# Optimization experiments

Hardware: AMD Instinct MI355X
Metric: run time of the kernel (lower is better)

Reference implementation:

```python
import jax, jax.numpy as jnp
import numpy as np

H = 256  # hidden_size


def _lstm_cell(x, h, c, Wih, Whh, b):
    # PyTorch gate order: input, forget, cell(g), output
    gates = x @ Wih.T + h @ Whh.T + b  # (B, 4H)
    i, f, g, o = jnp.split(gates, 4, axis=-1)
    c_new = jax.nn.sigmoid(f) * c + jax.nn.sigmoid(i) * jnp.tanh(g)
    h_new = jax.nn.sigmoid(o) * jnp.tanh(c_new)
    return h_new, c_new


def setup_inputs() -> dict:
    key = jax.random.key(0)
    ks = jax.random.split(key, 9)
    B, D_in, T, H4 = 64, 64, 1024, 4 * H
    s = 0.05  # keep gates out of saturation
    return {
        "x": jax.random.normal(ks[0], (B, D_in, T), jnp.float32),
        # layer 0: input size 64; layers 1-2: input size 2*H (bidirectional concat)
        "Wih0": jax.random.normal(ks[1], (2, H4, D_in), jnp.float32) * s,
        "Whh0": jax.random.normal(ks[2], (2, H4, H), jnp.float32) * s,
        "b0": jax.random.normal(ks[3], (2, H4), jnp.float32) * s,  # b_ih + b_hh fused
        "Wih12": jax.random.normal(ks[4], (2, 2, H4, 2 * H), jnp.float32) * s,
        "Whh12": jax.random.normal(ks[5], (2, 2, H4, H), jnp.float32) * s,
        "b12": jax.random.normal(ks[6], (2, 2, H4), jnp.float32) * s,
        # Conv1d(1, 81, (256,1)) == per-timestep linear over the hidden dim
        "conv_w": jax.random.normal(ks[7], (81, H), jnp.float32) * s,
        "conv_b": jax.random.normal(ks[8], (81,), jnp.float32) * s,
    }


def reference(x, Wih0, Whh0, b0, Wih12, Whh12, b12, conv_w, conv_b):
    B = x.shape[0]
    seq = jnp.transpose(x, (2, 0, 1))  # (T, B, D_in) like x.permute(2,0,1)
    h0 = jnp.zeros((6, B, H), x.dtype)  # num_layers * num_directions = 6
    c0 = jnp.zeros((6, B, H), x.dtype)

    def step(carry, x_t):
        h, c = carry
        hs, cs = [], []
        inp = x_t  # single timestep fed to the (bi)LSTM: both dirs see the same input
        for l in range(3):
            outs = []
            for d in range(2):
                idx = 2 * l + d
                if l == 0:
                    Wih, Whh, b = Wih0[d], Whh0[d], b0[d]
                else:
                    Wih, Whh, b = Wih12[l - 1, d], Whh12[l - 1, d], b12[l - 1, d]
                hn, cn = _lstm_cell(inp, h[idx], c[idx], Wih, Whh, b)
                outs.append(hn)
                hs.append(hn)
                cs.append(cn)
            inp = jnp.concatenate(outs, axis=-1)  # (B, 2H) into next layer
        new_h = jnp.stack(hs)
        new_c = jnp.stack(cs)
        # h.view(L, 2, B, H)[-1, -1]: last layer, backward direction
        return (new_h, new_c), hs[-1]

    _, ys = jax.lax.scan(step, (h0, c0), seq)  # ys: (T, B, H)

    # y.permute(1,2,0).unsqueeze(1) -> conv (256,1) kernel -> squeeze(2):
    # logits[b, o, t] = sum_h conv_w[o, h] * ys[t, b, h] + conv_b[o]
    logits = jnp.einsum('tbh,oh->bot', ys, conv_w) + conv_b[None, :, None]
    probs = jax.nn.softmax(logits, axis=1)
    return jnp.argmax(probs, axis=1)  # (B, T) int
```

## Files before the change

kernel.cpp:

```cpp
#include <hip/hip_runtime.h>


#define H_ 256
#define B_ 64
#define T_ 1024
#define NBLK 256
#define NTHR 1024
#define HBUF 98304
#define NTICK 1026

#define OFF_GEN  0
#define OFF_ROOT 64
#define OFF_CNT  128
#define OFF_H    4096
#define OFF_XT   1048576
#define OFF_YS   17825792

__device__ __forceinline__ float sigf(float x) {
  return 1.0f / (1.0f + __expf(-x));
}
__device__ __forceinline__ float tanhf_(float x) {
  float e = __expf(-2.0f * fabsf(x));
  float r = (1.0f - e) / (1.0f + e);
  return x >= 0.0f ? r : -r;
}

__device__ __forceinline__ void llc_ld1(const float4* p, float4& r) {
  asm volatile(
      "global_load_dwordx4 %0, %1, off sc0 sc1\n\t"
      "s_waitcnt vmcnt(0)"
      : "=v"(r)
      : "v"(p)
      : "memory");
}
__device__ __forceinline__ void llc_ld4(const float4* p, float4& r0, float4& r1,
                                        float4& r2, float4& r3) {
  asm volatile(
      "global_load_dwordx4 %0, %4, off sc0 sc1\n\t"
      "global_load_dwordx4 %1, %4, off offset:1024 sc0 sc1\n\t"
      "global_load_dwordx4 %2, %4, off offset:2048 sc0 sc1\n\t"
      "global_load_dwordx4 %3, %4, off offset:3072 sc0 sc1\n\t"
      "s_waitcnt vmcnt(0)"
      : "=&v"(r0), "=&v"(r1), "=&v"(r2), "=&v"(r3)
      : "v"(p)
      : "memory");
}
__device__ __forceinline__ void llc_st1(float* p, float v) {
  asm volatile(
      "global_store_dword %0, %1, off sc0 sc1\n\t"
      "s_waitcnt vmcnt(0)" ::"v"(p),
      "v"(v)
      : "memory");
}
__device__ __forceinline__ void llc_st2(float* p1, float v1, float* p2, float v2) {
  asm volatile(
      "global_store_dword %0, %1, off sc0 sc1\n\t"
      "global_store_dword %2, %3, off sc0 sc1\n\t"
      "s_waitcnt vmcnt(0)" ::"v"(p1),
      "v"(v1), "v"(p2), "v"(v2)
      : "memory");
}

__global__ __launch_bounds__(64) void transpose_x(const float* __restrict__ x,
                                                  float* __restrict__ xT) {
  __shared__ float tile[64][65];
  const int k = blockIdx.y;
  const int t0 = blockIdx.x * 64;
  const int lane = threadIdx.x;
  for (int bi = 0; bi < 64; ++bi)
    tile[bi][lane] = x[bi * 65536 + k * 1024 + t0 + lane];
  __syncthreads();
  for (int ti = 0; ti < 64; ++ti)
    xT[(size_t)(t0 + ti) * 4096 + (k >> 2) * 256 + lane * 4 + (k & 3)] =
        tile[lane][ti];
}

__device__ __forceinline__ void body8(float* __restrict__ acc, const float4 av,
                                      const float* __restrict__ wl,
                                      const int k4) {
  const float* wp = wl + (size_t)k4 * 32;
#pragma unroll
  for (int a = 0; a < 8; ++a) {
    float4 wq = *(const float4*)(wp + a * 4);
    acc[a] += wq.x * av.x + wq.y * av.y + wq.z * av.z + wq.w * av.w;
  }
}

__device__ __forceinline__ void seg8(float* __restrict__ acc, const int a,
                                     const int b, const float4* __restrict__ act,
                                     const int actOff,
                                     const float* __restrict__ wl,
                                     const int lane, const bool byp) {
  int k4 = a;
  for (; k4 + 4 <= b; k4 += 4) {
    const float4* p = act + (size_t)(k4 - actOff) * 64 + lane;
    float4 v0, v1, v2, v3;
    if (byp) {
      llc_ld4(p, v0, v1, v2, v3);
    } else {
      v0 = p[0];
      v1 = p[64];
      v2 = p[128];
      v3 = p[192];
    }
    body8(acc, v0, wl, k4 + 0);
    body8(acc, v1, wl, k4 + 1);
    body8(acc, v2, wl, k4 + 2);
    body8(acc, v3, wl, k4 + 3);
  }
  for (; k4 < b; ++k4) {
    const float4* p = act + (size_t)(k4 - actOff) * 64 + lane;
    float4 v;
    if (byp)
      llc_ld1(p, v);
    else
      v = *p;
    body8(acc, v, wl, k4);
  }
}

__device__ __forceinline__ void task8(
    const int w, const int lane, const int tid, const int u0,
    const int K4, const int nA4,
    const float4* __restrict__ actA, const bool bypA,
    const float4* __restrict__ actB, const bool bypB,
    const float* __restrict__ wl,
    const float* __restrict__ bias,
    float* __restrict__ cst2,
    float* __restrict__ hcell,
    float* __restrict__ ysrow,
    float (*red)[64][12], const bool lastTask) {
  const int slice = K4 >> 4;
  const int lo = w * slice, hi = lo + slice;
  float acc[8] = {0.f, 0.f, 0.f, 0.f, 0.f, 0.f, 0.f, 0.f};

  {
    const int b4 = hi < nA4 ? hi : nA4;
    if (lo < b4) seg8(acc, lo, b4, actA, 0, wl, lane, bypA);
  }
  {
    const int a4 = lo > nA4 ? lo : nA4;
    if (a4 < hi) seg8(acc, a4, hi, actB, nA4, wl, lane, bypB);
  }

  *(float4*)&red[w][lane][0] = make_float4(acc[0], acc[1], acc[2], acc[3]);
  *(float4*)&red[w][lane][4] = make_float4(acc[4], acc[5], acc[6], acc[7]);
  __syncthreads();

  if (tid < 128) {
    const int uu = tid >> 6, b = tid & 63;
    float gi = bias[0 * 256 + u0 + uu];
    float gf = bias[1 * 256 + u0 + uu];
    float gg = bias[2 * 256 + u0 + uu];
    float go = bias[3 * 256 + u0 + uu];
#pragma unroll
    for (int ww = 0; ww < 16; ++ww) {
      float4 s = *(const float4*)&red[ww][b][uu * 4];
      gi += s.x; gf += s.y; gg += s.z; go += s.w;
    }
    float iv = sigf(gi), fv = sigf(gf), gv = tanhf_(gg), ov = sigf(go);
    float c = fv * cst2[uu * 64 + b] + iv * gv;
    cst2[uu * 64 + b] = c;
    float h = ov * tanhf_(c);
    const int u = u0 + uu;
    float* hp = hcell + (u >> 2) * 256 + b * 4 + (u & 3);
    if (ysrow)
      llc_st2(hp, h, ysrow + b * 256 + u, h);
    else
      llc_st1(hp, h);
  }
  if (!lastTask) __syncthreads();
}

__global__ __launch_bounds__(NTHR, 1) void lstm_persistent(
    const float* __restrict__ Wih0, const float* __restrict__ Whh0,
    const float* __restrict__ b0, const float* __restrict__ Wih12,
    const float* __restrict__ Whh12, const float* __restrict__ b12, char* wsb) {
  unsigned* gen = (unsigned*)(wsb + OFF_GEN);
  unsigned* root = (unsigned*)(wsb + OFF_ROOT);
  float* hb = (float*)(wsb + OFF_H);
  const float* xT = (const float*)(wsb + OFF_XT);
  float* ys = (float*)(wsb + OFF_YS);

  __shared__ float red[16][64][12];
  __shared__ float cst[3][2][64];
  __shared__ float wlds[14848];

  const int bid = blockIdx.x;
  const int tid = threadIdx.x;
  const int lane = tid & 63;
  const int w = __builtin_amdgcn_readfirstlane(tid >> 6);
  const int d = bid >> 7;
  const int u0 = (bid & 127) * 2;

  if (tid < 384) ((float*)cst)[tid] = 0.f;

  auto stage = [&](const float* wA, int wAs, const float* wB, int wBs,
                   int K4s, int NA4s, float* dst) {
    const int nq = K4s * 8;
    for (int idx = tid; idx < nq; idx += NTHR) {
      const int a = idx / K4s;
      const int k4 = idx - a * K4s;
      const int row = (a & 3) * 256 + u0 + (a >> 2);
      const float* src = (k4 < NA4s) ? (wA + (size_t)row * wAs + k4 * 4)
                                     : (wB + (size_t)row * wBs + (k4 - NA4s) * 4);
      float4 q = *(const float4*)src;
      *(float4*)(dst + ((size_t)k4 * 8 + a) * 4) = q;
    }
  };
  stage(Wih0 + (size_t)d * 65536, 64, Whh0 + (size_t)d * 262144, 256, 80, 16,
        wlds);
  stage(Wih12 + (size_t)d * 524288, 512, Whh12 + (size_t)d * 262144, 256, 192,
        128, wlds + 2560);
  stage(Wih12 + (size_t)(2 + d) * 524288, 512,
        Whh12 + (size_t)(2 + d) * 262144, 256, 192, 128, wlds + 8704);
  __syncthreads();

  unsigned* mycnt = (unsigned*)(wsb + OFF_CNT + (size_t)(bid & 7) * 64);

  for (unsigned tick = 0; tick < NTICK; ++tick) {
    const float* R = hb + ((tick + 1) & 1) * HBUF;
    float* W = hb + (tick & 1) * HBUF;
    const float4* Rf4 = (const float4*)R;

    const bool has0 = tick < 1024;
    const bool has1 = tick >= 1 && tick < 1025;
    const bool has2 = tick >= 2;

    if (has0) {
      task8(w, lane, tid, u0, 80, 16,
            (const float4*)xT + (size_t)tick * 1024, false,
            Rf4 + (size_t)d * 4096, true,
            wlds, b0 + d * 1024, &cst[0][0][0],
            W + (size_t)d * 16384, nullptr, red, !(has1 || has2));
    }
    if (has1) {
      task8(w, lane, tid, u0, 192, 128,
            Rf4, true,
            Rf4 + (size_t)(2 + d) * 4096, true,
            wlds + 2560, b12 + d * 1024, &cst[1][0][0],
            W + (size_t)(2 + d) * 16384, nullptr, red, !has2);
    }
    if (has2) {
      const int t = (int)tick - 2;
      task8(w, lane, tid, u0, 192, 128,
            Rf4 + (size_t)2 * 4096, true,
            Rf4 + (size_t)(4 + d) * 4096, true,
            wlds + 8704, b12 + (2 + d) * 1024, &cst[2][0][0],
            W + (size_t)(4 + d) * 16384,
            (d == 1) ? (ys + (size_t)t * 16384) : nullptr, red, true);
    }

    __syncthreads();
    if (tid == 0) {
      unsigned old = __hip_atomic_fetch_add(mycnt, 1u, __ATOMIC_RELAXED,
                                            __HIP_MEMORY_SCOPE_AGENT);
      if (old == (tick + 1) * (NBLK / 8) - 1) {
        unsigned r = __hip_atomic_fetch_add(root, 1u, __ATOMIC_RELAXED,
                                            __HIP_MEMORY_SCOPE_AGENT);
        if (r == (tick + 1) * 8 - 1) {
          __hip_atomic_store(gen, tick + 1, __ATOMIC_RELAXED,
                             __HIP_MEMORY_SCOPE_AGENT);
        }
      }
      while (__hip_atomic_load(gen, __ATOMIC_RELAXED, __HIP_MEMORY_SCOPE_AGENT) <
             tick + 1) {
        __builtin_amdgcn_s_sleep(2);
      }
    }
    __syncthreads();
  }
}

__global__ __launch_bounds__(256) void conv_argmax(const float* __restrict__ yst,
                                                   const float* __restrict__ cw,
                                                   const float* __restrict__ cb,
                                                   int* __restrict__ out) {
  const int t = blockIdx.x;
  const int tid = threadIdx.x, lane = tid & 63, w = tid >> 6;
  const float* yrow = yst + (size_t)t * (B_ * H_) + lane * H_;
  float best = -3.4e38f;
  int bi = 0;
  for (int og = 0; og < 3; ++og) {
    float acc[8];
    int ov[8];
#pragma unroll
    for (int m = 0; m < 8; ++m) {
      int o = w + 32 * og + 4 * m;
      ov[m] = (o < 81) ? o : 80;
      acc[m] = (o < 81) ? cb[o] : -3.4e38f;
    }
    for (int uu = 0; uu < H_; uu += 4) {
      float4 y4 = *(const float4*)(yrow + uu);
#pragma unroll
      for (int m = 0; m < 8; ++m) {
        const float* wr = cw + ov[m] * H_ + uu;
        acc[m] += wr[0] * y4.x + wr[1] * y4.y + wr[2] * y4.z + wr[3] * y4.w;
      }
    }
#pragma unroll
    for (int m = 0; m < 8; ++m) {
      int o = w + 32 * og + 4 * m;
      if (o < 81 && acc[m] > best) {
        best = acc[m];
        bi = o;
      }
    }
  }
  __shared__ float sv[4][64];
  __shared__ int si[4][64];
  sv[w][lane] = best;
  si[w][lane] = bi;
  __syncthreads();
  if (tid < 64) {
    float bv = sv[0][tid];
    int bo = si[0][tid];
#pragma unroll
    for (int ww = 1; ww < 4; ++ww) {
      float v = sv[ww][tid];
      int o = si[ww][tid];
      if (v > bv || (v == bv && o < bo)) {
        bv = v;
        bo = o;
      }
    }
    out[tid * T_ + t] = bo;
  }
}

extern "C" void kernel_launch(void* const* d_in, const int* in_sizes, int n_in,
                              void* d_out, int out_size, void* d_ws,
                              size_t ws_size, hipStream_t stream) {
  const float* x = (const float*)d_in[0];
  const float* Wih0 = (const float*)d_in[1];
  const float* Whh0 = (const float*)d_in[2];
  const float* b0 = (const float*)d_in[3];
  const float* Wih12 = (const float*)d_in[4];
  const float* Whh12 = (const float*)d_in[5];
  const float* b12 = (const float*)d_in[6];
  const float* cw = (const float*)d_in[7];
  const float* cb = (const float*)d_in[8];
  int* out = (int*)d_out;
  char* wsb = (char*)d_ws;

  hipMemsetAsync(wsb, 0, OFF_H + 786432, stream);
  transpose_x<<<dim3(16, 64, 1), dim3(64, 1, 1), 0, stream>>>(
      x, (float*)(wsb + OFF_XT));
  lstm_persistent<<<dim3(NBLK, 1, 1), dim3(NTHR, 1, 1), 0, stream>>>(
      Wih0, Whh0, b0, Wih12, Whh12, b12, wsb);
  conv_argmax<<<dim3(T_, 1, 1), dim3(256, 1, 1), 0, stream>>>(
      (const float*)(wsb + OFF_YS), cw, cb, out);
}
```

Measured before the change: 18.34 ms.

## Run three LSTM layer cells concurrently across warp groups per tick

Instead of running the three layer cells one after another, each with its own block-wide reduction and barrier, the 16 warps are split into groups: 4 for layer 0 and 6 each for layers 1 and 2. All three matvecs now run at once, followed by a single shared reduction and pointwise phase handled by 192 threads. This removes two __syncthreads per tick and shortens the serial per-tick path. It also adds 8-wide bypass loads, caches the biases in LDS, and packs the two hidden-unit stores into one dwordx2 store. The cost is uneven work per warp, since layer-0 warps have less K to cover.

```diff
diff --git a/kernel.cpp b/kernel.cpp
--- a/kernel.cpp
+++ b/kernel.cpp
@@ -45,20 +45,28 @@
       : "v"(p)
       : "memory");
 }
-__device__ __forceinline__ void llc_st1(float* p, float v) {
+__device__ __forceinline__ void llc_ld8(const float4* p, const float4* q,
+                                        float4& r0, float4& r1, float4& r2,
+                                        float4& r3, float4& r4, float4& r5,
+                                        float4& r6, float4& r7) {
   asm volatile(
-      "global_store_dword %0, %1, off sc0 sc1\n\t"
-      "s_waitcnt vmcnt(0)" ::"v"(p),
-      "v"(v)
+      "global_load_dwordx4 %0, %8, off sc0 sc1\n\t"
+      "global_load_dwordx4 %1, %8, off offset:1024 sc0 sc1\n\t"
+      "global_load_dwordx4 %2, %8, off offset:2048 sc0 sc1\n\t"
+      "global_load_dwordx4 %3, %8, off offset:3072 sc0 sc1\n\t"
+      "global_load_dwordx4 %4, %9, off sc0 sc1\n\t"
+      "global_load_dwordx4 %5, %9, off offset:1024 sc0 sc1\n\t"
+      "global_load_dwordx4 %6, %9, off offset:2048 sc0 sc1\n\t"
+      "global_load_dwordx4 %7, %9, off offset:3072 sc0 sc1\n\t"
+      "s_waitcnt vmcnt(0)"
+      : "=&v"(r0), "=&v"(r1), "=&v"(r2), "=&v"(r3), "=&v"(r4), "=&v"(r5),
+        "=&v"(r6), "=&v"(r7)
+      : "v"(p), "v"(q)
       : "memory");
 }
-__device__ __forceinline__ void llc_st2(float* p1, float v1, float* p2, float v2) {
-  asm volatile(
-      "global_store_dword %0, %1, off sc0 sc1\n\t"
-      "global_store_dword %2, %3, off sc0 sc1\n\t"
-      "s_waitcnt vmcnt(0)" ::"v"(p1),
-      "v"(v1), "v"(p2), "v"(v2)
-      : "memory");
+__device__ __forceinline__ void llc_st_f2(float* p, float2 v) {
+  asm volatile("global_store_dwordx2 %0, %1, off sc0 sc1" ::"v"(p), "v"(v)
+               : "memory");
 }
 
 __global__ __launch_bounds__(64) void transpose_x(const float* __restrict__ x,
@@ -86,90 +94,65 @@
   }
 }
 
-__device__ __forceinline__ void seg8(float* __restrict__ acc, const int a,
-                                     const int b, const float4* __restrict__ act,
-                                     const int actOff,
-                                     const float* __restrict__ wl,
-                                     const int lane, const bool byp) {
-  int k4 = a;
-  for (; k4 + 4 <= b; k4 += 4) {
-    const float4* p = act + (size_t)(k4 - actOff) * 64 + lane;
+__device__ __forceinline__ void runLLC(float* __restrict__ acc,
+                                       const float4* __restrict__ bufbase,
+                                       const int bufk4, const int wk4,
+                                       const int n,
+                                       const float* __restrict__ wl,
+                                       const int lane) {
+  const float4* p = bufbase + (size_t)bufk4 * 64 + lane;
+  int k = 0;
+  for (; k + 8 <= n; k += 8) {
+    float4 v0, v1, v2, v3, v4, v5, v6, v7;
+    llc_ld8(p, p + 256, v0, v1, v2, v3, v4, v5, v6, v7);
+    p += 512;
+    body8(acc, v0, wl, wk4 + k + 0);
+    body8(acc, v1, wl, wk4 + k + 1);
+    body8(acc, v2, wl, wk4 + k + 2);
+    body8(acc, v3, wl, wk4 + k + 3);
+    body8(acc, v4, wl, wk4 + k + 4);
+    body8(acc, v5, wl, wk4 + k + 5);
+    body8(acc, v6, wl, wk4 + k + 6);
+    body8(acc, v7, wl, wk4 + k + 7);
+  }
+  for (; k + 4 <= n; k += 4) {
     float4 v0, v1, v2, v3;
-    if (byp) {
-      llc_ld4(p, v0, v1, v2, v3);
-    } else {
-      v0 = p[0];
-      v1 = p[64];
-      v2 = p[128];
-      v3 = p[192];
-    }
-    body8(acc, v0, wl, k4 + 0);
-    body8(acc, v1, wl, k4 + 1);
-    body8(acc, v2, wl, k4 + 2);
-    body8(acc, v3, wl, k4 + 3);
-  }
-  for (; k4 < b; ++k4) {
-    const float4* p = act + (size_t)(k4 - actOff) * 64 + lane;
+    llc_ld4(p, v0, v1, v2, v3);
+    p += 256;
+    body8(acc, v0, wl, wk4 + k + 0);
+    body8(acc, v1, wl, wk4 + k + 1);
+    body8(acc, v2, wl, wk4 + k + 2);
+    body8(acc, v3, wl, wk4 + k + 3);
+  }
+  for (; k < n; ++k) {
     float4 v;
-    if (byp)
-      llc_ld1(p, v);
-    else
-      v = *p;
-    body8(acc, v, wl, k4);
-  }
-}
-
-__device__ __forceinline__ void task8(
-    const int w, const int lane, const int tid, const int u0,
-    const int K4, const int nA4,
-    const float4* __restrict__ actA, const bool bypA,
-    const float4* __restrict__ actB, const bool bypB,
-    const float* __restrict__ wl,
-    const float* __restrict__ bias,
-    float* __restrict__ cst2,
-    float* __restrict__ hcell,
-    float* __restrict__ ysrow,
-    float (*red)[64][12], const bool lastTask) {
-  const int slice = K4 >> 4;
-  const int lo = w * slice, hi = lo + slice;
-  float acc[8] = {0.f, 0.f, 0.f, 0.f, 0.f, 0.f, 0.f, 0.f};
-
-  {
-    const int b4 = hi < nA4 ? hi : nA4;
-    if (lo < b4) seg8(acc, lo, b4, actA, 0, wl, lane, bypA);
-  }
-  {
-    const int a4 = lo > nA4 ? lo : nA4;
-    if (a4 < hi) seg8(acc, a4, hi, actB, nA4, wl, lane, bypB);
-  }
-
-  *(float4*)&red[w][lane][0] = make_float4(acc[0], acc[1], acc[2], acc[3]);
-  *(float4*)&red[w][lane][4] = make_float4(acc[4], acc[5], acc[6], acc[7]);
-  __syncthreads();
-
-  if (tid < 128) {
-    const int uu = tid >> 6, b = tid & 63;
-    float gi = bias[0 * 256 + u0 + uu];
-    float gf = bias[1 * 256 + u0 + uu];
-    float gg = bias[2 * 256 + u0 + uu];
-    float go = bias[3 * 256 + u0 + uu];
-#pragma unroll
-    for (int ww = 0; ww < 16; ++ww) {
-      float4 s = *(const float4*)&red[ww][b][uu * 4];
-      gi += s.x; gf += s.y; gg += s.z; go += s.w;
-    }
-    float iv = sigf(gi), fv = sigf(gf), gv = tanhf_(gg), ov = sigf(go);
-    float c = fv * cst2[uu * 64 + b] + iv * gv;
-    cst2[uu * 64 + b] = c;
-    float h = ov * tanhf_(c);
-    const int u = u0 + uu;
-    float* hp = hcell + (u >> 2) * 256 + b * 4 + (u & 3);
-    if (ysrow)
-      llc_st2(hp, h, ysrow + b * 256 + u, h);
-    else
-      llc_st1(hp, h);
-  }
-  if (!lastTask) __syncthreads();
+    llc_ld1(p, v);
+    p += 64;
+    body8(acc, v, wl, wk4 + k);
+  }
+}
+
+__device__ __forceinline__ void runCached(float* __restrict__ acc,
+                                          const float4* __restrict__ bufbase,
+                                          const int bufk4, const int wk4,
+                                          const int n,
+                                          const float* __restrict__ wl,
+                                          const int lane) {
+  const float4* p = bufbase + (size_t)bufk4 * 64 + lane;
+  int k = 0;
+  for (; k + 4 <= n; k += 4) {
+    float4 v0 = p[0], v1 = p[64], v2 = p[128], v3 = p[192];
+    p += 256;
+    body8(acc, v0, wl, wk4 + k + 0);
+    body8(acc, v1, wl, wk4 + k + 1);
+    body8(acc, v2, wl, wk4 + k + 2);
+    body8(acc, v3, wl, wk4 + k + 3);
+  }
+  for (; k < n; ++k) {
+    float4 v = *p;
+    p += 64;
+    body8(acc, v, wl, wk4 + k);
+  }
 }
 
 __global__ __launch_bounds__(NTHR, 1) void lstm_persistent(
@@ -185,6 +168,7 @@
   __shared__ float red[16][64][12];
   __shared__ float cst[3][2][64];
   __shared__ float wlds[14848];
+  __shared__ float blds[3][8];
 
   const int bid = blockIdx.x;
   const int tid = threadIdx.x;
@@ -214,6 +198,13 @@
         128, wlds + 2560);
   stage(Wih12 + (size_t)(2 + d) * 524288, 512,
         Whh12 + (size_t)(2 + d) * 262144, 256, 192, 128, wlds + 8704);
+  if (tid < 24) {
+    const int cell = tid >> 3, a = tid & 7;
+    const float* bb = (cell == 0) ? (b0 + d * 1024)
+                                  : ((cell == 1) ? (b12 + d * 1024)
+                                                 : (b12 + (2 + d) * 1024));
+    blds[cell][a] = bb[(a & 3) * 256 + u0 + (a >> 2)];
+  }
   __syncthreads();
 
   unsigned* mycnt = (unsigned*)(wsb + OFF_CNT + (size_t)(bid & 7) * 64);
@@ -227,31 +218,80 @@
     const bool has1 = tick >= 1 && tick < 1025;
     const bool has2 = tick >= 2;
 
-    if (has0) {
-      task8(w, lane, tid, u0, 80, 16,
-            (const float4*)xT + (size_t)tick * 1024, false,
-            Rf4 + (size_t)d * 4096, true,
-            wlds, b0 + d * 1024, &cst[0][0][0],
-            W + (size_t)d * 16384, nullptr, red, !(has1 || has2));
-    }
-    if (has1) {
-      task8(w, lane, tid, u0, 192, 128,
-            Rf4, true,
-            Rf4 + (size_t)(2 + d) * 4096, true,
-            wlds + 2560, b12 + d * 1024, &cst[1][0][0],
-            W + (size_t)(2 + d) * 16384, nullptr, red, !has2);
-    }
-    if (has2) {
-      const int t = (int)tick - 2;
-      task8(w, lane, tid, u0, 192, 128,
-            Rf4 + (size_t)2 * 4096, true,
-            Rf4 + (size_t)(4 + d) * 4096, true,
-            wlds + 8704, b12 + (2 + d) * 1024, &cst[2][0][0],
-            W + (size_t)(4 + d) * 16384,
-            (d == 1) ? (ys + (size_t)t * 16384) : nullptr, red, true);
-    }
-
+    float acc[8] = {0.f, 0.f, 0.f, 0.f, 0.f, 0.f, 0.f, 0.f};
+
+    if (w < 4) {
+      if (has0) {
+        if (w == 0) {
+          runCached(acc, (const float4*)xT + (size_t)tick * 1024, 0, 0, 16,
+                    wlds, lane);
+          runLLC(acc, Rf4 + (size_t)d * 4096, 0, 16, 4, wlds, lane);
+        } else {
+          const int lo = 20 * w;
+          runLLC(acc, Rf4 + (size_t)d * 4096, lo - 16, lo, 20, wlds, lane);
+        }
+      }
+    } else if (w < 10) {
+      if (has1) {
+        const int wi = w - 4, lo = 32 * wi;
+        if (wi < 4)
+          runLLC(acc, Rf4, lo, lo, 32, wlds + 2560, lane);
+        else
+          runLLC(acc, Rf4 + (size_t)(2 + d) * 4096, lo - 128, lo, 32,
+                 wlds + 2560, lane);
+      }
+    } else {
+      if (has2) {
+        const int wi = w - 10, lo = 32 * wi;
+        if (wi < 4)
+          runLLC(acc, Rf4 + (size_t)2 * 4096, lo, lo, 32, wlds + 8704, lane);
+        else
+          runLLC(acc, Rf4 + (size_t)(4 + d) * 4096, lo - 128, lo, 32,
+                 wlds + 8704, lane);
+      }
+    }
+
+    *(float4*)&red[w][lane][0] = make_float4(acc[0], acc[1], acc[2], acc[3]);
+    *(float4*)&red[w][lane][4] = make_float4(acc[4], acc[5], acc[6], acc[7]);
     __syncthreads();
+
+    if (tid < 192) {
+      const int cell = tid >> 6, b = tid & 63;
+      const bool present = (cell == 0) ? has0 : ((cell == 1) ? has1 : has2);
+      if (present) {
+        const int w0 = (cell == 0) ? 0 : ((cell == 1) ? 4 : 10);
+        const int nw = (cell == 0) ? 4 : 6;
+        float g0 = blds[cell][0], g1 = blds[cell][1], g2 = blds[cell][2],
+              g3 = blds[cell][3], g4 = blds[cell][4], g5 = blds[cell][5],
+              g6 = blds[cell][6], g7 = blds[cell][7];
+        for (int ww = w0; ww < w0 + nw; ++ww) {
+          const float4* rp = (const float4*)&red[ww][b][0];
+          float4 s0 = rp[0], s1 = rp[1];
+          g0 += s0.x; g1 += s0.y; g2 += s0.z; g3 += s0.w;
+          g4 += s1.x; g5 += s1.y; g6 += s1.z; g7 += s1.w;
+        }
+        const float iv0 = sigf(g0), fv0 = sigf(g1), gv0 = tanhf_(g2),
+                    ov0 = sigf(g3);
+        const float iv1 = sigf(g4), fv1 = sigf(g5), gv1 = tanhf_(g6),
+                    ov1 = sigf(g7);
+        float c0 = fv0 * cst[cell][0][b] + iv0 * gv0;
+        float c1 = fv1 * cst[cell][1][b] + iv1 * gv1;
+        cst[cell][0][b] = c0;
+        cst[cell][1][b] = c1;
+        const float h0 = ov0 * tanhf_(c0), h1 = ov1 * tanhf_(c1);
+        const int cellidx = (cell == 0) ? d : ((cell == 1) ? (2 + d) : (4 + d));
+        float* hp =
+            W + (size_t)cellidx * 16384 + (u0 >> 2) * 256 + b * 4 + (u0 & 3);
+        llc_st_f2(hp, make_float2(h0, h1));
+        if (cell == 2 && d == 1) {
+          *(float2*)(ys + (size_t)((int)tick - 2) * 16384 + b * 256 + u0) =
+              make_float2(h0, h1);
+        }
+      }
+    }
+    asm volatile("s_waitcnt vmcnt(0)" ::: "memory");
+    __syncthreads();
+
     if (tid == 0) {
       unsigned old = __hip_atomic_fetch_add(mycnt, 1u, __ATOMIC_RELAXED,
                                             __HIP_MEMORY_SCOPE_AGENT);
```

New measurement: 16.13 ms, median of 2. -12.1%, faster.
